# Kernel tuning notes

Measured on AMD Instinct MI355X. Metric: run time of the kernel, lower is better.

## Reference

```python
import jax, jax.numpy as jnp
import numpy as np

B, S, E, H, A = 2, 1024, 1024, 16, 3
HD = E // H

def setup_inputs() -> dict:
    key = jax.random.key(0)
    ks = jax.random.split(key, 8)
    return {
        "query": jax.random.normal(ks[0], (B, S, E), dtype=jnp.float32),
        "key": jax.random.normal(ks[1], (B, S, E), dtype=jnp.float32),
        "value": jax.random.normal(ks[2], (B, S, E), dtype=jnp.float32),
        "aid": jax.random.normal(ks[3], (B, S, S, A), dtype=jnp.float32),
        "mixer_w": jax.random.uniform(ks[4], (H, A + 1, 1), dtype=jnp.float32),
        "mixer_b": jax.random.uniform(ks[5], (H, 1), dtype=jnp.float32),
        "Wo": jax.random.normal(ks[6], (E, E), dtype=jnp.float32) * 0.02,
        "bo": jax.random.normal(ks[7], (E,), dtype=jnp.float32) * 0.02,
        "aid_scale": jnp.array([0.1], dtype=jnp.float32),
    }

def reference(query, key, value, aid, mixer_w, mixer_b, Wo, bo, aid_scale):
    scale = HD ** -0.5
    # Faithful to source: raw row-major reshape (B,S,E)->(B,H,S,HD)
    q = query.reshape(B, H, S, HD)
    k = key.reshape(B, H, S, HD)
    v = value.reshape(B, H, S, HD)
    attn = jnp.einsum('bhqd,bhkd->bhqk', q, k) * scale  # (B,H,S,S)
    aid_h = jnp.broadcast_to(aid[:, None], (B, H, S, S, A))
    mix_in = jnp.concatenate([attn[..., None], aid_h], axis=-1)  # (B,H,S,S,A+1)
    mixed = jnp.einsum('bhqki,hio->bhqko', mix_in, mixer_w) + mixer_b[None, :, None, None, :]
    mixed = jax.nn.relu(mixed)[..., 0]  # (B,H,S,S)
    attn = attn + mixed * aid_scale[0]
    pre_softmax_attn = attn
    attn = jax.nn.softmax(attn, axis=-1)
    out = jnp.einsum('bhqk,bhkd->bhqd', attn, v)
    out = out.transpose(0, 2, 1, 3).reshape(B, S, E)
    out = out @ Wo.T + bo
    return out, attn, pre_softmax_attn
```

## Files before the change

### kernel.cpp

```cpp
#include <hip/hip_runtime.h>
#include <hip/hip_bf16.h>

using u16 = unsigned short;
typedef __attribute__((ext_vector_type(8))) short short8;
typedef __attribute__((ext_vector_type(4))) float f32x4;

constexpr int Bc = 2, Sc = 1024, Ec = 1024, Hc = 16, HDc = 64;
constexpr float SCALE = 0.125f;

__device__ __forceinline__ u16 f2bf(float f) {
    union { float f; unsigned u; } v{f};
    unsigned r = v.u + 0x7FFF + ((v.u >> 16) & 1);
    return (u16)(r >> 16);
}
__device__ __forceinline__ float bf2f(u16 x) {
    union { unsigned u; float f; } v; v.u = ((unsigned)x) << 16; return v.f;
}

__global__ __launch_bounds__(256) void k_convT(const float* __restrict__ V,
                                               u16* __restrict__ Vt) {
    __shared__ float tile[64][65];
    const int bh = blockIdx.y;
    const int k0 = blockIdx.x * 64;
    const float* Vp = V + (size_t)bh * Sc * HDc + (size_t)k0 * HDc;
    const int tid = threadIdx.x;

    #pragma unroll
    for (int it = 0; it < 4; ++it) {
        int idx = tid + it * 256;
        int k = idx >> 4, d4 = idx & 15;
        float4 v = *(const float4*)&Vp[k * HDc + d4 * 4];
        tile[d4 * 4 + 0][k] = v.x;
        tile[d4 * 4 + 1][k] = v.y;
        tile[d4 * 4 + 2][k] = v.z;
        tile[d4 * 4 + 3][k] = v.w;
    }
    __syncthreads();

    u16* Op = Vt + (size_t)bh * HDc * Sc + k0;
    #pragma unroll
    for (int it = 0; it < 4; ++it) {
        int idx = tid + it * 256;
        int d = idx >> 4, kq = idx & 15;
        u16 t[4];
        #pragma unroll
        for (int j = 0; j < 4; ++j) t[j] = f2bf(tile[d][kq * 4 + j]);
        *(uint2*)&Op[(size_t)d * Sc + kq * 4] = *(uint2*)t;
    }
}

__global__ __launch_bounds__(256, 2) void k_scores(
    const float* __restrict__ Qf, const float* __restrict__ Kf,
    const float* __restrict__ aid, const float* __restrict__ mw,
    const float* __restrict__ mb, const float* __restrict__ ascale,
    float* __restrict__ pre)
{
    __shared__ u16 Qs[64 * 64];
    __shared__ u16 Ks[64 * 64];

    const int bid = blockIdx.x;
    const int kt = bid & 15;
    const int qt = (bid >> 4) & 15;
    const int b  = bid >> 8;

    const int tid = threadIdx.x;
    const int w = tid >> 6, lane = tid & 63;
    const int lrow = lane & 15, lhi = lane >> 4;

    float a3[4][4][3];
    #pragma unroll
    for (int r = 0; r < 4; ++r) {
        const size_t qg = (size_t)(b * Sc + qt * 64 + w * 16 + lhi * 4 + r) * Sc;
        #pragma unroll
        for (int fk = 0; fk < 4; ++fk) {
            const float* ap = aid + (qg + kt * 64 + fk * 16 + lrow) * 3;
            float2 t2 = *(const float2*)ap;
            a3[r][fk][0] = t2.x; a3[r][fk][1] = t2.y; a3[r][fk][2] = ap[2];
        }
    }

    const float asc = ascale[0];
    const float* Qbase = Qf + ((size_t)b * Hc * Sc + qt * 64) * HDc;
    const float* Kbase = Kf + ((size_t)b * Hc * Sc + kt * 64) * HDc;

    for (int h = 0; h < Hc; ++h) {
        const float* Qp = Qbase + (size_t)h * Sc * HDc;
        const float* Kp = Kbase + (size_t)h * Sc * HDc;
        #pragma unroll
        for (int it = 0; it < 2; ++it) {
            int idx = tid + it * 256;
            int r = idx >> 3, g = idx & 7;
            int gs = (g ^ (r & 7)) * 8;
            const float* qs = Qp + r * 64 + g * 8;
            const float* ks = Kp + r * 64 + g * 8;
            float4 qa = *(const float4*)qs, qb = *(const float4*)(qs + 4);
            float4 ka = *(const float4*)ks, kb = *(const float4*)(ks + 4);
            u16 tq[8] = {f2bf(qa.x), f2bf(qa.y), f2bf(qa.z), f2bf(qa.w),
                         f2bf(qb.x), f2bf(qb.y), f2bf(qb.z), f2bf(qb.w)};
            u16 tk[8] = {f2bf(ka.x), f2bf(ka.y), f2bf(ka.z), f2bf(ka.w),
                         f2bf(kb.x), f2bf(kb.y), f2bf(kb.z), f2bf(kb.w)};
            *(short8*)&Qs[r * 64 + gs] = *(short8*)tq;
            *(short8*)&Ks[r * 64 + gs] = *(short8*)tk;
        }
        __syncthreads();

        f32x4 acc[4] = {};
        #pragma unroll
        for (int ks2 = 0; ks2 < 2; ++ks2) {
            const int rq = w * 16 + lrow;
            short8 af = *(const short8*)&Qs[rq * 64 + ((ks2 * 4 + lhi) ^ (rq & 7)) * 8];
            #pragma unroll
            for (int fk = 0; fk < 4; ++fk) {
                const int rk = fk * 16 + lrow;
                short8 bf = *(const short8*)&Ks[rk * 64 + ((ks2 * 4 + lhi) ^ (rk & 7)) * 8];
                acc[fk] = __builtin_amdgcn_mfma_f32_16x16x32_bf16(af, bf, acc[fk], 0, 0, 0);
            }
        }

        const float w0 = mw[h * 4 + 0], w1 = mw[h * 4 + 1];
        const float w2 = mw[h * 4 + 2], w3 = mw[h * 4 + 3];
        const float bias = mb[h];
        float* prow0 = pre + ((size_t)(b * Hc + h) * Sc + qt * 64 + w * 16 + lhi * 4) * Sc
                     + kt * 64 + lrow;
        #pragma unroll
        for (int r = 0; r < 4; ++r) {
            #pragma unroll
            for (int fk = 0; fk < 4; ++fk) {
                float s = acc[fk][r] * SCALE;
                float mm = s * w0 + a3[r][fk][0] * w1 + a3[r][fk][1] * w2
                         + a3[r][fk][2] * w3 + bias;
                prow0[(size_t)r * Sc + fk * 16] = s + fmaxf(mm, 0.f) * asc;
            }
        }
        __syncthreads();
    }
}

__global__ __launch_bounds__(512, 1) void k_spv(
    const float* __restrict__ pre, const u16* __restrict__ Vt,
    float* __restrict__ attn, u16* __restrict__ Omid)
{
    __shared__ u16 band[64 * 1024];
    __shared__ u16 Vs[2][64 * 64];
    __shared__ float s_m[64], s_l[64];

    const int bid = blockIdx.x;
    const int bh  = bid >> 4;
    const int qt  = (bid & 15) * 64;
    const int b   = bh >> 4, h = bh & 15;

    const int tid  = threadIdx.x;
    const int w    = tid >> 6, lane = tid & 63;
    const int lrow = lane & 15, lhi = lane >> 4;

    const int arow_i = tid >> 3;
    const int sub    = tid & 7;
    const int asw    = arow_i & 7;
    const float* prow = pre + ((size_t)bh * Sc + qt + arow_i) * Sc;
    float m = -1e30f;
    #pragma unroll 4
    for (int kt = 0; kt < 16; ++kt) {
        const float* p0 = prow + kt * 64 + sub * 8;
        float s[8];
        *(float4*)&s[0] = *(const float4*)p0;
        *(float4*)&s[4] = *(const float4*)(p0 + 4);
        u16 t[8];
        #pragma unroll
        for (int j = 0; j < 8; ++j) { m = fmaxf(m, s[j]); t[j] = f2bf(s[j]); }
        *(short8*)&band[arow_i * 1024 + (kt * 8 + (sub ^ asw)) * 8] = *(short8*)t;
    }
    m = fmaxf(m, __shfl_xor(m, 1));
    m = fmaxf(m, __shfl_xor(m, 2));
    m = fmaxf(m, __shfl_xor(m, 4));
    if (sub == 0) s_m[arow_i] = m;

    const u16* Vp = Vt + (size_t)bh * HDc * Sc;
    {
        int r = tid >> 3, g = tid & 7;
        *(short8*)&Vs[0][r * 64 + (g ^ (r & 7)) * 8] =
            *(const short8*)&Vp[(size_t)r * Sc + g * 8];
    }
    __syncthreads();

    const int rf = w >> 1, dh = w & 1;
    const int brow = rf * 16 + lrow;
    const int bsw  = brow & 7;
    const float mreg = s_m[brow];
    float l = 0.f;
    f32x4 acc[2] = {};

    for (int kt = 0; kt < 16; ++kt) {
        if (kt < 15) {
            int r = tid >> 3, g = tid & 7;
            *(short8*)&Vs[(kt + 1) & 1][r * 64 + (g ^ (r & 7)) * 8] =
                *(const short8*)&Vp[(size_t)r * Sc + (kt + 1) * 64 + g * 8];
        }
        short8 ra = *(const short8*)&band[brow * 1024 + (kt * 8 + (lhi ^ bsw)) * 8];
        short8 rb = *(const short8*)&band[brow * 1024 + (kt * 8 + ((lhi + 4) ^ bsw)) * 8];
        u16 ea[8], eb[8];
        #pragma unroll
        for (int j = 0; j < 8; ++j) {
            float va = __expf(bf2f((u16)ra[j]) - mreg); l += va; ea[j] = f2bf(va);
            float vb = __expf(bf2f((u16)rb[j]) - mreg); l += vb; eb[j] = f2bf(vb);
        }
        const u16* vbuf = Vs[kt & 1];
        short8 A0 = *(short8*)ea, A1 = *(short8*)eb;
        #pragma unroll
        for (int fd = 0; fd < 2; ++fd) {
            int rv = dh * 32 + fd * 16 + lrow;
            short8 b0 = *(const short8*)&vbuf[rv * 64 + ((lhi) ^ (rv & 7)) * 8];
            short8 b1 = *(const short8*)&vbuf[rv * 64 + ((lhi + 4) ^ (rv & 7)) * 8];
            acc[fd] = __builtin_amdgcn_mfma_f32_16x16x32_bf16(A0, b0, acc[fd], 0, 0, 0);
            acc[fd] = __builtin_amdgcn_mfma_f32_16x16x32_bf16(A1, b1, acc[fd], 0, 0, 0);
        }
        __syncthreads();
    }
    l += __shfl_xor(l, 16);
    l += __shfl_xor(l, 32);
    if (dh == 0 && lhi == 0) s_l[brow] = l;
    __syncthreads();

    const float mf  = s_m[arow_i];
    const float inv = 1.f / s_l[arow_i];
    float* arow = attn + ((size_t)bh * Sc + qt + arow_i) * Sc;
    #pragma unroll 4
    for (int kt = 0; kt < 16; ++kt) {
        short8 ra = *(const short8*)&band[arow_i * 1024 + (kt * 8 + (sub ^ asw)) * 8];
        float o[8];
        #pragma unroll
        for (int j = 0; j < 8; ++j) o[j] = __expf(bf2f((u16)ra[j]) - mf) * inv;
        *(float4*)&arow[kt * 64 + sub * 8]     = *(float4*)&o[0];
        *(float4*)&arow[kt * 64 + sub * 8 + 4] = *(float4*)&o[4];
    }

    #pragma unroll
    for (int reg = 0; reg < 4; ++reg) {
        const int rowO = rf * 16 + lhi * 4 + reg;
        const float linv = 1.f / s_l[rowO];
        u16* orow = Omid + ((size_t)b * Sc + qt + rowO) * Ec + h * HDc + dh * 32;
        #pragma unroll
        for (int fd = 0; fd < 2; ++fd)
            orow[fd * 16 + lrow] = f2bf(acc[fd][reg] * linv);
    }
}

__global__ __launch_bounds__(256, 2) void k_proj(
    const u16* __restrict__ Ob, const float* __restrict__ Wof,
    const float* __restrict__ bo, float* __restrict__ out)
{
    __shared__ u16 Xs[128 * 64];
    __shared__ u16 Ws[64 * 64];

    const int bid = blockIdx.x;
    const int mt = (bid >> 4) * 128;
    const int et = (bid & 15) * 64;

    const int tid = threadIdx.x;
    const int w = tid >> 6, lane = tid & 63;
    const int lrow = lane & 15, lhi = lane >> 4;

    f32x4 acc[2][4] = {};

    for (int kb = 0; kb < Ec; kb += 64) {
        #pragma unroll
        for (int it = 0; it < 4; ++it) {
            int idx = tid + it * 256;
            int r = idx >> 3, g = idx & 7;
            *(short8*)&Xs[r * 64 + (g ^ (r & 7)) * 8] =
                *(const short8*)&Ob[(size_t)(mt + r) * Ec + kb + g * 8];
        }
        #pragma unroll
        for (int it = 0; it < 2; ++it) {
            int idx = tid + it * 256;
            int r = idx >> 3, g = idx & 7;
            const float* sp = &Wof[(size_t)(et + r) * Ec + kb + g * 8];
            float4 x = *(const float4*)sp, y = *(const float4*)(sp + 4);
            u16 t[8] = {f2bf(x.x), f2bf(x.y), f2bf(x.z), f2bf(x.w),
                        f2bf(y.x), f2bf(y.y), f2bf(y.z), f2bf(y.w)};
            *(short8*)&Ws[r * 64 + (g ^ (r & 7)) * 8] = *(short8*)t;
        }
        __syncthreads();

        #pragma unroll
        for (int ks = 0; ks < 2; ++ks) {
            short8 af[2], bfr[4];
            int g = ks * 4 + lhi;
            #pragma unroll
            for (int fq = 0; fq < 2; ++fq) {
                int rq = w * 32 + fq * 16 + lrow;
                af[fq] = *(const short8*)&Xs[rq * 64 + (g ^ (rq & 7)) * 8];
            }
            #pragma unroll
            for (int fd = 0; fd < 4; ++fd) {
                int rv = fd * 16 + lrow;
                bfr[fd] = *(const short8*)&Ws[rv * 64 + (g ^ (rv & 7)) * 8];
            }
            #pragma unroll
            for (int fq = 0; fq < 2; ++fq)
                #pragma unroll
                for (int fd = 0; fd < 4; ++fd)
                    acc[fq][fd] = __builtin_amdgcn_mfma_f32_16x16x32_bf16(
                        af[fq], bfr[fd], acc[fq][fd], 0, 0, 0);
        }
        __syncthreads();
    }

    #pragma unroll
    for (int fq = 0; fq < 2; ++fq)
        #pragma unroll
        for (int r = 0; r < 4; ++r) {
            const int m = mt + w * 32 + fq * 16 + lhi * 4 + r;
            float* orow = out + (size_t)m * Ec + et;
            #pragma unroll
            for (int fd = 0; fd < 4; ++fd) {
                int e = fd * 16 + lrow;
                orow[e] = acc[fq][fd][r] + bo[et + e];
            }
        }
}

extern "C" void kernel_launch(void* const* d_in, const int* in_sizes, int n_in,
                              void* d_out, int out_size, void* d_ws, size_t ws_size,
                              hipStream_t stream) {
    const float* query  = (const float*)d_in[0];
    const float* key    = (const float*)d_in[1];
    const float* value  = (const float*)d_in[2];
    const float* aid    = (const float*)d_in[3];
    const float* mw     = (const float*)d_in[4];
    const float* mb     = (const float*)d_in[5];
    const float* Wo     = (const float*)d_in[6];
    const float* bo     = (const float*)d_in[7];
    const float* ascale = (const float*)d_in[8];

    float* out_p  = (float*)d_out;
    float* attn_p = out_p + (size_t)Bc * Sc * Ec;
    float* pre_p  = attn_p + (size_t)Bc * Hc * Sc * Sc;

    u16* Vtb  = (u16*)d_ws;
    u16* Omid = Vtb + (size_t)2 * 1024 * 1024;

    k_convT<<<dim3(Sc / 64, Bc * Hc), 256, 0, stream>>>(value, Vtb);
    k_scores<<<Bc * 16 * 16, 256, 0, stream>>>(query, key, aid, mw, mb, ascale, pre_p);
    k_spv<<<512, 512, 0, stream>>>(pre_p, Vtb, attn_p, Omid);
    k_proj<<<(Bc * Sc / 128) * (Ec / 64), 256, 0, stream>>>(Omid, Wo, bo, out_p);
}
```

Measured before the change: 157.7 us.

## Pre-convert Q, K, Wo to bf16 once and read V directly from global

```diff
diff --git a/kernel.cpp b/kernel.cpp
--- a/kernel.cpp
+++ b/kernel.cpp
@@ -15,6 +15,24 @@
 }
 __device__ __forceinline__ float bf2f(u16 x) {
     union { unsigned u; float f; } v; v.u = ((unsigned)x) << 16; return v.f;
+}
+
+__global__ __launch_bounds__(256) void k_prep(
+    const float* __restrict__ Q, const float* __restrict__ K,
+    const float* __restrict__ Wo, u16* __restrict__ Qb,
+    u16* __restrict__ Kb, u16* __restrict__ Wob)
+{
+    const int bid = blockIdx.x;
+    const float* src; u16* dst; int base;
+    if (bid < 1024)      { src = Q;  dst = Qb;  base = bid; }
+    else if (bid < 2048) { src = K;  dst = Kb;  base = bid - 1024; }
+    else                 { src = Wo; dst = Wob; base = bid - 2048; }
+    const int i = (base * 256 + threadIdx.x) * 8;
+    float4 a = *(const float4*)&src[i];
+    float4 b = *(const float4*)&src[i + 4];
+    u16 t[8] = {f2bf(a.x), f2bf(a.y), f2bf(a.z), f2bf(a.w),
+                f2bf(b.x), f2bf(b.y), f2bf(b.z), f2bf(b.w)};
+    *(short8*)&dst[i] = *(short8*)t;
 }
 
 __global__ __launch_bounds__(256) void k_convT(const float* __restrict__ V,
@@ -50,7 +68,7 @@
 }
 
 __global__ __launch_bounds__(256, 2) void k_scores(
-    const float* __restrict__ Qf, const float* __restrict__ Kf,
+    const u16* __restrict__ Qb, const u16* __restrict__ Kb,
     const float* __restrict__ aid, const float* __restrict__ mw,
     const float* __restrict__ mb, const float* __restrict__ ascale,
     float* __restrict__ pre)
@@ -80,27 +98,19 @@
     }
 
     const float asc = ascale[0];
-    const float* Qbase = Qf + ((size_t)b * Hc * Sc + qt * 64) * HDc;
-    const float* Kbase = Kf + ((size_t)b * Hc * Sc + kt * 64) * HDc;
+    const u16* Qbase = Qb + ((size_t)b * Hc * Sc + qt * 64) * HDc;
+    const u16* Kbase = Kb + ((size_t)b * Hc * Sc + kt * 64) * HDc;
 
     for (int h = 0; h < Hc; ++h) {
-        const float* Qp = Qbase + (size_t)h * Sc * HDc;
-        const float* Kp = Kbase + (size_t)h * Sc * HDc;
+        const u16* Qp = Qbase + (size_t)h * Sc * HDc;
+        const u16* Kp = Kbase + (size_t)h * Sc * HDc;
         #pragma unroll
         for (int it = 0; it < 2; ++it) {
             int idx = tid + it * 256;
             int r = idx >> 3, g = idx & 7;
             int gs = (g ^ (r & 7)) * 8;
-            const float* qs = Qp + r * 64 + g * 8;
-            const float* ks = Kp + r * 64 + g * 8;
-            float4 qa = *(const float4*)qs, qb = *(const float4*)(qs + 4);
-            float4 ka = *(const float4*)ks, kb = *(const float4*)(ks + 4);
-            u16 tq[8] = {f2bf(qa.x), f2bf(qa.y), f2bf(qa.z), f2bf(qa.w),
-                         f2bf(qb.x), f2bf(qb.y), f2bf(qb.z), f2bf(qb.w)};
-            u16 tk[8] = {f2bf(ka.x), f2bf(ka.y), f2bf(ka.z), f2bf(ka.w),
-                         f2bf(kb.x), f2bf(kb.y), f2bf(kb.z), f2bf(kb.w)};
-            *(short8*)&Qs[r * 64 + gs] = *(short8*)tq;
-            *(short8*)&Ks[r * 64 + gs] = *(short8*)tk;
+            *(short8*)&Qs[r * 64 + gs] = *(const short8*)&Qp[r * 64 + g * 8];
+            *(short8*)&Ks[r * 64 + gs] = *(const short8*)&Kp[r * 64 + g * 8];
         }
         __syncthreads();
 
@@ -141,7 +151,6 @@
     float* __restrict__ attn, u16* __restrict__ Omid)
 {
     __shared__ u16 band[64 * 1024];
-    __shared__ u16 Vs[2][64 * 64];
     __shared__ float s_m[64], s_l[64];
 
     const int bid = blockIdx.x;
@@ -173,28 +182,18 @@
     m = fmaxf(m, __shfl_xor(m, 2));
     m = fmaxf(m, __shfl_xor(m, 4));
     if (sub == 0) s_m[arow_i] = m;
-
-    const u16* Vp = Vt + (size_t)bh * HDc * Sc;
-    {
-        int r = tid >> 3, g = tid & 7;
-        *(short8*)&Vs[0][r * 64 + (g ^ (r & 7)) * 8] =
-            *(const short8*)&Vp[(size_t)r * Sc + g * 8];
-    }
     __syncthreads();
 
     const int rf = w >> 1, dh = w & 1;
     const int brow = rf * 16 + lrow;
     const int bsw  = brow & 7;
     const float mreg = s_m[brow];
+    const u16* Vbase = Vt + (size_t)bh * HDc * Sc;
     float l = 0.f;
     f32x4 acc[2] = {};
 
+    #pragma unroll 4
     for (int kt = 0; kt < 16; ++kt) {
-        if (kt < 15) {
-            int r = tid >> 3, g = tid & 7;
-            *(short8*)&Vs[(kt + 1) & 1][r * 64 + (g ^ (r & 7)) * 8] =
-                *(const short8*)&Vp[(size_t)r * Sc + (kt + 1) * 64 + g * 8];
-        }
         short8 ra = *(const short8*)&band[brow * 1024 + (kt * 8 + (lhi ^ bsw)) * 8];
         short8 rb = *(const short8*)&band[brow * 1024 + (kt * 8 + ((lhi + 4) ^ bsw)) * 8];
         u16 ea[8], eb[8];
@@ -203,17 +202,16 @@
             float va = __expf(bf2f((u16)ra[j]) - mreg); l += va; ea[j] = f2bf(va);
             float vb = __expf(bf2f((u16)rb[j]) - mreg); l += vb; eb[j] = f2bf(vb);
         }
-        const u16* vbuf = Vs[kt & 1];
         short8 A0 = *(short8*)ea, A1 = *(short8*)eb;
         #pragma unroll
         for (int fd = 0; fd < 2; ++fd) {
-            int rv = dh * 32 + fd * 16 + lrow;
-            short8 b0 = *(const short8*)&vbuf[rv * 64 + ((lhi) ^ (rv & 7)) * 8];
-            short8 b1 = *(const short8*)&vbuf[rv * 64 + ((lhi + 4) ^ (rv & 7)) * 8];
+            const int rv = dh * 32 + fd * 16 + lrow;
+            const u16* vp = Vbase + (size_t)rv * Sc + kt * 64;
+            short8 b0 = *(const short8*)&vp[lhi * 8];
+            short8 b1 = *(const short8*)&vp[(lhi + 4) * 8];
             acc[fd] = __builtin_amdgcn_mfma_f32_16x16x32_bf16(A0, b0, acc[fd], 0, 0, 0);
             acc[fd] = __builtin_amdgcn_mfma_f32_16x16x32_bf16(A1, b1, acc[fd], 0, 0, 0);
         }
-        __syncthreads();
     }
     l += __shfl_xor(l, 16);
     l += __shfl_xor(l, 32);
@@ -245,7 +243,7 @@
 }
 
 __global__ __launch_bounds__(256, 2) void k_proj(
-    const u16* __restrict__ Ob, const float* __restrict__ Wof,
+    const u16* __restrict__ Ob, const u16* __restrict__ Wob,
     const float* __restrict__ bo, float* __restrict__ out)
 {
     __shared__ u16 Xs[128 * 64];
@@ -273,11 +271,8 @@
         for (int it = 0; it < 2; ++it) {
             int idx = tid + it * 256;
             int r = idx >> 3, g = idx & 7;
-            const float* sp = &Wof[(size_t)(et + r) * Ec + kb + g * 8];
-            float4 x = *(const float4*)sp, y = *(const float4*)(sp + 4);
-            u16 t[8] = {f2bf(x.x), f2bf(x.y), f2bf(x.z), f2bf(x.w),
-                        f2bf(y.x), f2bf(y.y), f2bf(y.z), f2bf(y.w)};
-            *(short8*)&Ws[r * 64 + (g ^ (r & 7)) * 8] = *(short8*)t;
+            *(short8*)&Ws[r * 64 + (g ^ (r & 7)) * 8] =
+                *(const short8*)&Wob[(size_t)(et + r) * Ec + kb + g * 8];
         }
         __syncthreads();
 
@@ -337,10 +332,14 @@
     float* pre_p  = attn_p + (size_t)Bc * Hc * Sc * Sc;
 
     u16* Vtb  = (u16*)d_ws;
-    u16* Omid = Vtb + (size_t)2 * 1024 * 1024;
-
+    u16* Omid = Vtb  + (size_t)2 * 1024 * 1024;
+    u16* Qb   = Omid + (size_t)2 * 1024 * 1024;
+    u16* Kb   = Qb   + (size_t)2 * 1024 * 1024;
+    u16* Wob  = Kb   + (size_t)2 * 1024 * 1024;
+
+    k_prep<<<2560, 256, 0, stream>>>(query, key, Wo, Qb, Kb, Wob);
     k_convT<<<dim3(Sc / 64, Bc * Hc), 256, 0, stream>>>(value, Vtb);
-    k_scores<<<Bc * 16 * 16, 256, 0, stream>>>(query, key, aid, mw, mb, ascale, pre_p);
+    k_scores<<<Bc * 16 * 16, 256, 0, stream>>>(Qb, Kb, aid, mw, mb, ascale, pre_p);
     k_spv<<<512, 512, 0, stream>>>(pre_p, Vtb, attn_p, Omid);
-    k_proj<<<(Bc * Sc / 128) * (Ec / 64), 256, 0, stream>>>(Omid, Wo, bo, out_p);
-}
+    k_proj<<<(Bc * Sc / 128) * (Ec / 64), 256, 0, stream>>>(Omid, Wob, bo, out_p);
+}
```

Result: faster. 147.9 us (-6.2%).
